# Kernel tuning notes

Hardware: AMD Instinct MI355X
Metric: run time of the kernel (lower is better)

The kernel has to match this reference:

```python
import jax, jax.numpy as jnp
import numpy as np

B, S, D, F, E, K = 2, 1024, 2048, 8192, 4, 2  # batch, seq, d_model, d_ff, n_experts, top_k


def setup_inputs() -> dict:
    key = jax.random.key(0)
    k0, k1, k2, k3, k4 = jax.random.split(key, 5)
    scaled = lambda k, shape, fan_in: (jax.random.normal(k, shape, jnp.float32) * (fan_in ** -0.5))
    return {
        "x": jax.random.normal(k0, (B, S, D), jnp.float32),
        "Wr": scaled(k1, (D, E), D),          # router (gating_layer.gate) weight
        "Wg": scaled(k2, (E, D, F), D),        # stacked expert gate_proj weights
        "Wu": scaled(k3, (E, D, F), D),        # stacked expert up_proj weights
        "Wd": scaled(k4, (E, F, D), F),        # stacked expert down_proj weights
    }


def reference(x, Wr, Wg, Wu, Wd):
    # Router: softmax over expert logits, take top-k values + indices
    probs = jax.nn.softmax(x @ Wr, axis=-1)                 # [B,S,E]
    gate_vals, gate_idx = jax.lax.top_k(probs, K)           # [B,S,K] each

    # Dense per-expert SwiGLU MLP for EVERY token (faithful to the original loop)
    g = jax.nn.silu(jnp.einsum('bsd,edf->bsef', x, Wg))     # [B,S,E,F]
    u = jnp.einsum('bsd,edf->bsef', x, Wu)                  # [B,S,E,F]
    eo = jnp.einsum('bsef,efd->bsed', g * u, Wd)            # [B,S,E,D]

    # Gather the top-k experts per token, scale by gate values, sum (combine)
    idx = jnp.broadcast_to(gate_idx[..., None], (B, S, K, D))
    sel = jnp.take_along_axis(eo, idx, axis=2)              # [B,S,K,D]
    return (sel * gate_vals[..., None]).sum(axis=2)         # [B,S,D]
```

## Files before the change

kernel.cpp:

```cpp
#include <hip/hip_runtime.h>
#include <stdint.h>


#define T_TOK 2048
#define DM    2048
#define FF    8192
#define DF    ((size_t)DM * FF)

typedef unsigned short u16;
typedef short short8 __attribute__((ext_vector_type(8)));
typedef float f32x4  __attribute__((ext_vector_type(4)));

#define GLL16(g, l) __builtin_amdgcn_global_load_lds( \
    (const __attribute__((address_space(1))) void*)(g), \
    (__attribute__((address_space(3))) void*)(l), 16, 0, 0)

__device__ __forceinline__ u16 f2bf(float f) {
  uint32_t x = __float_as_uint(f);
  x += 0x7fffu + ((x >> 16) & 1u);
  return (u16)(x >> 16);
}

__global__ __launch_bounds__(256) void router_kernel(
    const float* __restrict__ x, const float* __restrict__ Wr,
    int* __restrict__ counts, int* __restrict__ tok, float* __restrict__ gate)
{
  int t = blockIdx.x * 4 + (threadIdx.x >> 6);
  int l = threadIdx.x & 63;
  const float* xr = x + (size_t)t * DM;
  const float4* wr4 = (const float4*)Wr;
  float a0 = 0.f, a1 = 0.f, a2 = 0.f, a3 = 0.f;
  for (int d = l; d < DM; d += 64) {
    float xv = xr[d];
    float4 w = wr4[d];
    a0 += xv * w.x; a1 += xv * w.y; a2 += xv * w.z; a3 += xv * w.w;
  }
  #pragma unroll
  for (int off = 32; off > 0; off >>= 1) {
    a0 += __shfl_down(a0, off);
    a1 += __shfl_down(a1, off);
    a2 += __shfl_down(a2, off);
    a3 += __shfl_down(a3, off);
  }
  if (l == 0) {
    float lg[4] = {a0, a1, a2, a3};
    float m = fmaxf(fmaxf(lg[0], lg[1]), fmaxf(lg[2], lg[3]));
    float p[4], s = 0.f;
    #pragma unroll
    for (int e = 0; e < 4; ++e) { p[e] = __expf(lg[e] - m); s += p[e]; }
    #pragma unroll
    for (int e = 0; e < 4; ++e) p[e] /= s;
    int i0 = 0;
    #pragma unroll
    for (int e = 1; e < 4; ++e) if (p[e] > p[i0]) i0 = e;
    int i1 = (i0 == 0) ? 1 : 0;
    #pragma unroll
    for (int e = 0; e < 4; ++e) if (e != i0 && p[e] > p[i1]) i1 = e;
    int s0 = atomicAdd(&counts[i0], 1);
    tok[i0 * T_TOK + s0] = t; gate[i0 * T_TOK + s0] = p[i0];
    int s1 = atomicAdd(&counts[i1], 1);
    tok[i1 * T_TOK + s1] = t; gate[i1 * T_TOK + s1] = p[i1];
  }
}

__global__ __launch_bounds__(256) void gather_kernel(
    const float* __restrict__ x, const int* __restrict__ counts,
    const int* __restrict__ tok, u16* __restrict__ Xe)
{
  int e = blockIdx.x >> 11;
  int slot = blockIdx.x & (T_TOK - 1);
  if (slot >= counts[e]) return;
  int t = tok[e * T_TOK + slot];
  const float4* src = (const float4*)(x + (size_t)t * DM);
  u16* dst = Xe + ((size_t)e * T_TOK + slot) * DM;
  int i = threadIdx.x;
  float4 a = src[i * 2], b = src[i * 2 + 1];
  union { u16 h[8]; uint4 q; } v;
  v.h[0] = f2bf(a.x); v.h[1] = f2bf(a.y); v.h[2] = f2bf(a.z); v.h[3] = f2bf(a.w);
  v.h[4] = f2bf(b.x); v.h[5] = f2bf(b.y); v.h[6] = f2bf(b.z); v.h[7] = f2bf(b.w);
  *(uint4*)(dst + i * 8) = v.q;
}

__global__ __launch_bounds__(256) void trans_cvt_all(
    const float* __restrict__ Wg, const float* __restrict__ Wu, const float* __restrict__ Wd,
    u16* __restrict__ Wgt, u16* __restrict__ Wut, u16* __restrict__ Wdt)
{
  int j = blockIdx.y;
  const float* src; u16* dst; int R, C, clog;
  if (j < 4)      { src = Wg + (size_t)j * DF;       dst = Wgt + (size_t)j * DF;       R = DM; C = FF; clog = 7; }
  else if (j < 8) { src = Wu + (size_t)(j - 4) * DF; dst = Wut + (size_t)(j - 4) * DF; R = DM; C = FF; clog = 7; }
  else            { src = Wd + (size_t)(j - 8) * DF; dst = Wdt + (size_t)(j - 8) * DF; R = FF; C = DM; clog = 5; }
  int bx = blockIdx.x;
  int c0 = (bx & ((1 << clog) - 1)) * 64;
  int r0 = (bx >> clog) * 64;

  __shared__ float tile[64][65];
  int tid = threadIdx.x;
  int tc = tid & 63, tr = tid >> 6;
  #pragma unroll
  for (int i = 0; i < 16; ++i) {
    int row = i * 4 + tr;
    tile[row][tc] = src[(size_t)(r0 + row) * C + c0 + tc];
  }
  __syncthreads();
  int wr = tid & 15, rr = tid >> 4;
  #pragma unroll
  for (int i = 0; i < 4; ++i) {
    int row = i * 16 + rr;
    ushort4 v;
    v.x = f2bf(tile[wr * 4 + 0][row]);
    v.y = f2bf(tile[wr * 4 + 1][row]);
    v.z = f2bf(tile[wr * 4 + 2][row]);
    v.w = f2bf(tile[wr * 4 + 3][row]);
    *(ushort4*)&dst[(size_t)(c0 + row) * R + r0 + wr * 4] = v;
  }
}

__global__ __launch_bounds__(256, 2) void gemm12_kernel(
    const u16* __restrict__ XeB, const u16* __restrict__ WgtB, const u16* __restrict__ WutB,
    u16* __restrict__ HB, const int* __restrict__ counts)
{
  const int e  = blockIdx.y >> 4;
  const int rb = blockIdx.y & 15;
  const int cnt = counts[e];
  if (rb * 128 >= cnt) return;
  const u16* A  = XeB + (size_t)e * T_TOK * DM;
  const u16* Bg = WgtB + (size_t)e * DF;
  const u16* Bu = WutB + (size_t)e * DF;
  u16* H = HB + (size_t)e * T_TOK * FF;

  __shared__ __align__(16) u16 As[128 * 64];
  __shared__ __align__(16) u16 Bgs[128 * 64];
  __shared__ __align__(16) u16 Bus[128 * 64];
  const int tid = threadIdx.x, l = tid & 63, w = tid >> 6;
  const int wm = w & 1, wn = w >> 1;
  const int cg = (l & 7) ^ (l >> 3);
  const u16* ap[4]; const u16* bgp[4]; const u16* bup[4];
  const u16* la[4]; const u16* lbg[4]; const u16* lbu[4];
  #pragma unroll
  for (int j = 0; j < 4; ++j) {
    int r0 = (w * 4 + j) * 8;
    int row = r0 + (l >> 3);
    ap[j]  = A  + (size_t)(rb * 128 + row) * DM + cg * 8;
    bgp[j] = Bg + (size_t)(blockIdx.x * 128 + row) * DM + cg * 8;
    bup[j] = Bu + (size_t)(blockIdx.x * 128 + row) * DM + cg * 8;
    la[j]  = As  + r0 * 64;
    lbg[j] = Bgs + r0 * 64;
    lbu[j] = Bus + r0 * 64;
  }
  int fm[4], fn[4];
  #pragma unroll
  for (int i = 0; i < 4; ++i) {
    fm[i] = (wm * 64 + i * 16 + (l & 15)) * 64;
    fn[i] = (wn * 64 + i * 16 + (l & 15)) * 64;
  }
  f32x4 accg[4][4] = {};
  f32x4 accu[4][4] = {};
  for (int kt = 0; kt < DM / 64; ++kt) {
    #pragma unroll
    for (int j = 0; j < 4; ++j) {
      GLL16(ap[j]  + kt * 64, la[j]);
      GLL16(bgp[j] + kt * 64, lbg[j]);
      GLL16(bup[j] + kt * 64, lbu[j]);
    }
    __syncthreads();
    #pragma unroll
    for (int kk = 0; kk < 2; ++kk) {
      const int c2 = ((kk * 4 + (l >> 4)) ^ (l & 7)) * 8;
      short8 af[4], bgf[4], buf_[4];
      #pragma unroll
      for (int i = 0; i < 4; ++i) af[i]   = *(const short8*)&As[fm[i] + c2];
      #pragma unroll
      for (int i = 0; i < 4; ++i) bgf[i]  = *(const short8*)&Bgs[fn[i] + c2];
      #pragma unroll
      for (int i = 0; i < 4; ++i) buf_[i] = *(const short8*)&Bus[fn[i] + c2];
      #pragma unroll
      for (int mt = 0; mt < 4; ++mt)
        #pragma unroll
        for (int nt = 0; nt < 4; ++nt) {
          accg[mt][nt] = __builtin_amdgcn_mfma_f32_16x16x32_bf16(af[mt], bgf[nt],  accg[mt][nt], 0, 0, 0);
          accu[mt][nt] = __builtin_amdgcn_mfma_f32_16x16x32_bf16(af[mt], buf_[nt], accu[mt][nt], 0, 0, 0);
        }
    }
    __syncthreads();
  }
  const int rbase = rb * 128 + wm * 64 + ((l >> 4) << 2);
  const int cbase = blockIdx.x * 128 + wn * 64 + (l & 15);
  #pragma unroll
  for (int mt = 0; mt < 4; ++mt) {
    #pragma unroll
    for (int i = 0; i < 4; ++i) {
      int r = rbase + mt * 16 + i;
      u16* hrow = H + (size_t)r * FF + cbase;
      #pragma unroll
      for (int nt = 0; nt < 4; ++nt) {
        float g = accg[mt][nt][i], u = accu[mt][nt][i];
        float h = (g / (1.f + __expf(-g))) * u;
        hrow[nt * 16] = f2bf(h);
      }
    }
  }
}

__global__ __launch_bounds__(256, 2) void gemm3_kernel(
    const u16* __restrict__ HB, const u16* __restrict__ WdtB,
    float* __restrict__ out, const int* __restrict__ counts,
    const int* __restrict__ tokB, const float* __restrict__ gateB)
{
  const int e  = blockIdx.y >> 4;
  const int rb = blockIdx.y & 15;
  const int cnt = counts[e];
  if (rb * 128 >= cnt) return;
  const u16* A = HB + (size_t)e * T_TOK * FF;
  const u16* B = WdtB + (size_t)e * DF;
  const int* tokd = tokB + e * T_TOK;
  const float* gated = gateB + e * T_TOK;
  const int kt0 = blockIdx.z * 64, kt1 = kt0 + 64;

  __shared__ __align__(16) u16 As[128 * 64];
  __shared__ __align__(16) u16 Bs[128 * 64];
  const int tid = threadIdx.x, l = tid & 63, w = tid >> 6;
  const int wm = w & 1, wn = w >> 1;
  const int cg = (l & 7) ^ (l >> 3);
  const u16* ap[4]; const u16* bp[4]; const u16* la[4]; const u16* lb[4];
  #pragma unroll
  for (int j = 0; j < 4; ++j) {
    int r0 = (w * 4 + j) * 8;
    int row = r0 + (l >> 3);
    ap[j] = A + (size_t)(rb * 128 + row) * FF + cg * 8;
    bp[j] = B + (size_t)(blockIdx.x * 128 + row) * FF + cg * 8;
    la[j] = As + r0 * 64;
    lb[j] = Bs + r0 * 64;
  }
  int fm[4], fn[4];
  #pragma unroll
  for (int i = 0; i < 4; ++i) {
    fm[i] = (wm * 64 + i * 16 + (l & 15)) * 64;
    fn[i] = (wn * 64 + i * 16 + (l & 15)) * 64;
  }
  f32x4 acc[4][4] = {};
  for (int kt = kt0; kt < kt1; ++kt) {
    #pragma unroll
    for (int j = 0; j < 4; ++j) {
      GLL16(ap[j] + kt * 64, la[j]);
      GLL16(bp[j] + kt * 64, lb[j]);
    }
    __syncthreads();
    #pragma unroll
    for (int kk = 0; kk < 2; ++kk) {
      const int c2 = ((kk * 4 + (l >> 4)) ^ (l & 7)) * 8;
      short8 af[4], bf[4];
      #pragma unroll
      for (int i = 0; i < 4; ++i) af[i] = *(const short8*)&As[fm[i] + c2];
      #pragma unroll
      for (int i = 0; i < 4; ++i) bf[i] = *(const short8*)&Bs[fn[i] + c2];
      #pragma unroll
      for (int mt = 0; mt < 4; ++mt)
        #pragma unroll
        for (int nt = 0; nt < 4; ++nt)
          acc[mt][nt] = __builtin_amdgcn_mfma_f32_16x16x32_bf16(af[mt], bf[nt], acc[mt][nt], 0, 0, 0);
    }
    __syncthreads();
  }
  const int rbase = rb * 128 + wm * 64 + ((l >> 4) << 2);
  const int cbase = blockIdx.x * 128 + wn * 64 + (l & 15);
  #pragma unroll
  for (int mt = 0; mt < 4; ++mt) {
    #pragma unroll
    for (int i = 0; i < 4; ++i) {
      int r = rbase + mt * 16 + i;
      if (r < cnt) {
        int t = tokd[r];
        float gv = gated[r];
        float* orow = out + (size_t)t * DM + cbase;
        #pragma unroll
        for (int nt = 0; nt < 4; ++nt)
          atomicAdd(orow + nt * 16, acc[mt][nt][i] * gv);
      }
    }
  }
}

extern "C" void kernel_launch(void* const* d_in, const int* in_sizes, int n_in,
                              void* d_out, int out_size, void* d_ws, size_t ws_size,
                              hipStream_t stream) {
  (void)in_sizes; (void)n_in; (void)out_size; (void)ws_size;
  const float* x  = (const float*)d_in[0];
  const float* Wr = (const float*)d_in[1];
  const float* Wg = (const float*)d_in[2];
  const float* Wu = (const float*)d_in[3];
  const float* Wd = (const float*)d_in[4];
  float* out = (float*)d_out;

  char* ws = (char*)d_ws;
  int*   counts = (int*)(ws);
  int*   tok    = (int*)(ws + 1024);
  float* gate   = (float*)(ws + 1024 + 4 * T_TOK * 4);
  u16*   Xe     = (u16*)(ws + 1024 + 2 * 4 * T_TOK * 4);
  u16*   Wgt    = Xe  + (size_t)4 * T_TOK * DM;
  u16*   Wut    = Wgt + 4 * DF;
  u16*   Wdt    = Wut + 4 * DF;
  u16*   H      = Wdt + 4 * DF;

  hipMemsetAsync(out, 0, (size_t)T_TOK * DM * sizeof(float), stream);
  hipMemsetAsync(counts, 0, 4 * sizeof(int), stream);

  router_kernel<<<T_TOK / 4, 256, 0, stream>>>(x, Wr, counts, tok, gate);
  gather_kernel<<<4 * T_TOK, 256, 0, stream>>>(x, counts, tok, Xe);
  trans_cvt_all<<<dim3(4096, 12), 256, 0, stream>>>(Wg, Wu, Wd, Wgt, Wut, Wdt);
  gemm12_kernel<<<dim3(FF / 128, 64), 256, 0, stream>>>(Xe, Wgt, Wut, H, counts);
  gemm3_kernel<<<dim3(DM / 128, 64, 2), 256, 0, stream>>>(H, Wdt, out, counts, tok, gate);
}
```

Baseline: 1.333 ms.

## Triple-buffer GEMM LDS tiles with 8-wave blocks and vectorize weight transpose

```diff
diff --git a/kernel.cpp b/kernel.cpp
--- a/kernel.cpp
+++ b/kernel.cpp
@@ -14,6 +14,12 @@
 #define GLL16(g, l) __builtin_amdgcn_global_load_lds( \
     (const __attribute__((address_space(1))) void*)(g), \
     (__attribute__((address_space(3))) void*)(l), 16, 0, 0)
+
+#define BARRIER() do { asm volatile("" ::: "memory"); __builtin_amdgcn_s_barrier(); asm volatile("" ::: "memory"); } while (0)
+#define LGK0()    do { asm volatile("s_waitcnt lgkmcnt(0)" ::: "memory"); __builtin_amdgcn_sched_barrier(0); } while (0)
+#define VMW(N)    asm volatile("s_waitcnt vmcnt(" #N ")" ::: "memory")
+#define PRIO1()   __builtin_amdgcn_s_setprio(1)
+#define PRIO0()   __builtin_amdgcn_s_setprio(0)
 
 __device__ __forceinline__ u16 f2bf(float f) {
   uint32_t x = __float_as_uint(f);
@@ -94,29 +100,28 @@
   int c0 = (bx & ((1 << clog) - 1)) * 64;
   int r0 = (bx >> clog) * 64;
 
-  __shared__ float tile[64][65];
+  __shared__ float tile[64][68];
   int tid = threadIdx.x;
-  int tc = tid & 63, tr = tid >> 6;
-  #pragma unroll
-  for (int i = 0; i < 16; ++i) {
-    int row = i * 4 + tr;
-    tile[row][tc] = src[(size_t)(r0 + row) * C + c0 + tc];
+  const float4* s4 = (const float4*)(src + (size_t)r0 * C + c0);
+  const int cq = C >> 2;
+  #pragma unroll
+  for (int k2 = 0; k2 < 4; ++k2) {
+    int f = tid + 256 * k2;
+    int row = f >> 4, c4 = f & 15;
+    float4 v = s4[(size_t)row * cq + c4];
+    *(float4*)&tile[row][c4 * 4] = v;
   }
   __syncthreads();
-  int wr = tid & 15, rr = tid >> 4;
-  #pragma unroll
-  for (int i = 0; i < 4; ++i) {
-    int row = i * 16 + rr;
-    ushort4 v;
-    v.x = f2bf(tile[wr * 4 + 0][row]);
-    v.y = f2bf(tile[wr * 4 + 1][row]);
-    v.z = f2bf(tile[wr * 4 + 2][row]);
-    v.w = f2bf(tile[wr * 4 + 3][row]);
-    *(ushort4*)&dst[(size_t)(c0 + row) * R + r0 + wr * 4] = v;
-  }
-}
-
-__global__ __launch_bounds__(256, 2) void gemm12_kernel(
+  int ro = tid >> 2, seg = tid & 3;
+  union { u16 h[16]; uint4 q[2]; } v;
+  #pragma unroll
+  for (int i = 0; i < 16; ++i) v.h[i] = f2bf(tile[seg * 16 + i][ro]);
+  u16* drow = dst + (size_t)(c0 + ro) * R + r0 + seg * 16;
+  *(uint4*)(drow)     = v.q[0];
+  *(uint4*)(drow + 8) = v.q[1];
+}
+
+__global__ __launch_bounds__(512, 2) void gemm12_kernel(
     const u16* __restrict__ XeB, const u16* __restrict__ WgtB, const u16* __restrict__ WutB,
     u16* __restrict__ HB, const int* __restrict__ counts)
 {
@@ -124,85 +129,103 @@
   const int rb = blockIdx.y & 15;
   const int cnt = counts[e];
   if (rb * 128 >= cnt) return;
-  const u16* A  = XeB + (size_t)e * T_TOK * DM;
-  const u16* Bg = WgtB + (size_t)e * DF;
-  const u16* Bu = WutB + (size_t)e * DF;
+  const u16* Ag  = XeB  + (size_t)e * T_TOK * DM + (size_t)rb * 128 * DM;
+  const u16* Bgg = WgtB + (size_t)e * DF + (size_t)blockIdx.x * 128 * DM;
+  const u16* Bug = WutB + (size_t)e * DF + (size_t)blockIdx.x * 128 * DM;
   u16* H = HB + (size_t)e * T_TOK * FF;
 
-  __shared__ __align__(16) u16 As[128 * 64];
-  __shared__ __align__(16) u16 Bgs[128 * 64];
-  __shared__ __align__(16) u16 Bus[128 * 64];
+  __shared__ __align__(16) u16 ldsT[3][3][128 * 64];
+
   const int tid = threadIdx.x, l = tid & 63, w = tid >> 6;
   const int wm = w & 1, wn = w >> 1;
   const int cg = (l & 7) ^ (l >> 3);
-  const u16* ap[4]; const u16* bgp[4]; const u16* bup[4];
-  const u16* la[4]; const u16* lbg[4]; const u16* lbu[4];
-  #pragma unroll
-  for (int j = 0; j < 4; ++j) {
-    int r0 = (w * 4 + j) * 8;
-    int row = r0 + (l >> 3);
-    ap[j]  = A  + (size_t)(rb * 128 + row) * DM + cg * 8;
-    bgp[j] = Bg + (size_t)(blockIdx.x * 128 + row) * DM + cg * 8;
-    bup[j] = Bu + (size_t)(blockIdx.x * 128 + row) * DM + cg * 8;
-    la[j]  = As  + r0 * 64;
-    lbg[j] = Bgs + r0 * 64;
-    lbu[j] = Bus + r0 * 64;
-  }
-  int fm[4], fn[4];
-  #pragma unroll
-  for (int i = 0; i < 4; ++i) {
-    fm[i] = (wm * 64 + i * 16 + (l & 15)) * 64;
-    fn[i] = (wn * 64 + i * 16 + (l & 15)) * 64;
-  }
-  f32x4 accg[4][4] = {};
-  f32x4 accu[4][4] = {};
-  for (int kt = 0; kt < DM / 64; ++kt) {
-    #pragma unroll
-    for (int j = 0; j < 4; ++j) {
-      GLL16(ap[j]  + kt * 64, la[j]);
-      GLL16(bgp[j] + kt * 64, lbg[j]);
-      GLL16(bup[j] + kt * 64, lbu[j]);
-    }
-    __syncthreads();
-    #pragma unroll
-    for (int kk = 0; kk < 2; ++kk) {
-      const int c2 = ((kk * 4 + (l >> 4)) ^ (l & 7)) * 8;
-      short8 af[4], bgf[4], buf_[4];
+  const size_t so0 = (size_t)(w * 16 + (l >> 3)) * DM + cg * 8;
+  const size_t so1 = so0 + (size_t)8 * DM;
+  const int lo0 = w * 1024;
+  const int lo1 = lo0 + 512;
+
+  int fmA[4], fnB[2], c2k[2];
+  #pragma unroll
+  for (int m = 0; m < 4; ++m) fmA[m] = (wm * 64 + m * 16 + (l & 15)) * 64;
+  #pragma unroll
+  for (int n = 0; n < 2; ++n) fnB[n] = (wn * 32 + n * 16 + (l & 15)) * 64;
+  c2k[0] = ((l >> 4) ^ (l & 7)) * 8;
+  c2k[1] = ((4 + (l >> 4)) ^ (l & 7)) * 8;
+
+  f32x4 accg[4][2] = {};
+  f32x4 accu[4][2] = {};
+
+  #define G12_STAGE(ti, which, srcp) do { \
+    u16* d_ = &ldsT[(ti) % 3][which][0]; \
+    GLL16((srcp) + (size_t)(ti) * 64 + so0, d_ + lo0); \
+    GLL16((srcp) + (size_t)(ti) * 64 + so1, d_ + lo1); } while (0)
+
+  G12_STAGE(0, 0, Ag); G12_STAGE(0, 1, Bgg);
+  G12_STAGE(0, 2, Bug);
+  G12_STAGE(1, 0, Ag); G12_STAGE(1, 1, Bgg);
+  G12_STAGE(1, 2, Bug);
+  VMW(8);
+  BARRIER();
+
+  #define G12_KTILE(T, ISSUE, KA, KB) do { \
+    const u16* a_  = &ldsT[(T) % 3][0][0]; \
+    const u16* bg_ = &ldsT[(T) % 3][1][0]; \
+    const u16* bu_ = &ldsT[(T) % 3][2][0]; \
+    short8 af[2][4], bgf[2][2], buf2[2][2]; \
+    _Pragma("unroll") \
+    for (int kk = 0; kk < 2; ++kk) { \
+      _Pragma("unroll") \
+      for (int m = 0; m < 4; ++m) af[kk][m] = *(const short8*)&a_[fmA[m] + c2k[kk]]; \
+      _Pragma("unroll") \
+      for (int n = 0; n < 2; ++n) bgf[kk][n] = *(const short8*)&bg_[fnB[n] + c2k[kk]]; \
+    } \
+    if (ISSUE) { G12_STAGE((T) + 2, 0, Ag); G12_STAGE((T) + 2, 1, Bgg); } \
+    BARRIER(); LGK0(); PRIO1(); \
+    _Pragma("unroll") \
+    for (int kk = 0; kk < 2; ++kk) \
+      _Pragma("unroll") \
+      for (int m = 0; m < 4; ++m) \
+        _Pragma("unroll") \
+        for (int n = 0; n < 2; ++n) \
+          accg[m][n] = __builtin_amdgcn_mfma_f32_16x16x32_bf16(af[kk][m], bgf[kk][n], accg[m][n], 0, 0, 0); \
+    PRIO0(); VMW(KA); BARRIER(); \
+    _Pragma("unroll") \
+    for (int kk = 0; kk < 2; ++kk) { \
+      _Pragma("unroll") \
+      for (int n = 0; n < 2; ++n) buf2[kk][n] = *(const short8*)&bu_[fnB[n] + c2k[kk]]; \
+    } \
+    if (ISSUE) { G12_STAGE((T) + 2, 2, Bug); } \
+    BARRIER(); LGK0(); PRIO1(); \
+    _Pragma("unroll") \
+    for (int kk = 0; kk < 2; ++kk) \
+      _Pragma("unroll") \
+      for (int m = 0; m < 4; ++m) \
+        _Pragma("unroll") \
+        for (int n = 0; n < 2; ++n) \
+          accu[m][n] = __builtin_amdgcn_mfma_f32_16x16x32_bf16(af[kk][m], buf2[kk][n], accu[m][n], 0, 0, 0); \
+    PRIO0(); VMW(KB); BARRIER(); \
+  } while (0)
+
+  for (int t = 0; t < 30; ++t) G12_KTILE(t, 1, 10, 8);
+  G12_KTILE(30, 0, 6, 2);
+  G12_KTILE(31, 0, 0, 0);
+
+  const int rloc = rb * 128 + wm * 64 + ((l >> 4) << 2);
+  const int cb   = blockIdx.x * 128 + wn * 32 + (l & 15);
+  #pragma unroll
+  for (int m = 0; m < 4; ++m)
+    #pragma unroll
+    for (int i = 0; i < 4; ++i) {
+      u16* hrow = H + (size_t)(rloc + m * 16 + i) * FF + cb;
       #pragma unroll
-      for (int i = 0; i < 4; ++i) af[i]   = *(const short8*)&As[fm[i] + c2];
-      #pragma unroll
-      for (int i = 0; i < 4; ++i) bgf[i]  = *(const short8*)&Bgs[fn[i] + c2];
-      #pragma unroll
-      for (int i = 0; i < 4; ++i) buf_[i] = *(const short8*)&Bus[fn[i] + c2];
-      #pragma unroll
-      for (int mt = 0; mt < 4; ++mt)
-        #pragma unroll
-        for (int nt = 0; nt < 4; ++nt) {
-          accg[mt][nt] = __builtin_amdgcn_mfma_f32_16x16x32_bf16(af[mt], bgf[nt],  accg[mt][nt], 0, 0, 0);
-          accu[mt][nt] = __builtin_amdgcn_mfma_f32_16x16x32_bf16(af[mt], buf_[nt], accu[mt][nt], 0, 0, 0);
-        }
-    }
-    __syncthreads();
-  }
-  const int rbase = rb * 128 + wm * 64 + ((l >> 4) << 2);
-  const int cbase = blockIdx.x * 128 + wn * 64 + (l & 15);
-  #pragma unroll
-  for (int mt = 0; mt < 4; ++mt) {
-    #pragma unroll
-    for (int i = 0; i < 4; ++i) {
-      int r = rbase + mt * 16 + i;
-      u16* hrow = H + (size_t)r * FF + cbase;
-      #pragma unroll
-      for (int nt = 0; nt < 4; ++nt) {
-        float g = accg[mt][nt][i], u = accu[mt][nt][i];
-        float h = (g / (1.f + __expf(-g))) * u;
-        hrow[nt * 16] = f2bf(h);
+      for (int n = 0; n < 2; ++n) {
+        float g = accg[m][n][i], u = accu[m][n][i];
+        hrow[n * 16] = f2bf((g / (1.f + __expf(-g))) * u);
       }
     }
-  }
-}
-
-__global__ __launch_bounds__(256, 2) void gemm3_kernel(
+}
+
+__global__ __launch_bounds__(512, 2) void gemm3_kernel(
     const u16* __restrict__ HB, const u16* __restrict__ WdtB,
     float* __restrict__ out, const int* __restrict__ counts,
     const int* __restrict__ tokB, const float* __restrict__ gateB)
@@ -211,74 +234,93 @@
   const int rb = blockIdx.y & 15;
   const int cnt = counts[e];
   if (rb * 128 >= cnt) return;
-  const u16* A = HB + (size_t)e * T_TOK * FF;
-  const u16* B = WdtB + (size_t)e * DF;
+  const u16* Ag = HB   + (size_t)e * T_TOK * FF + (size_t)rb * 128 * FF;
+  const u16* Bgp = WdtB + (size_t)e * DF + (size_t)blockIdx.x * 256 * FF;
   const int* tokd = tokB + e * T_TOK;
   const float* gated = gateB + e * T_TOK;
-  const int kt0 = blockIdx.z * 64, kt1 = kt0 + 64;
-
-  __shared__ __align__(16) u16 As[128 * 64];
-  __shared__ __align__(16) u16 Bs[128 * 64];
+
+  __shared__ __align__(16) u16 ldsA[3][128 * 64];
+  __shared__ __align__(16) u16 ldsB[3][256 * 64];
+
   const int tid = threadIdx.x, l = tid & 63, w = tid >> 6;
   const int wm = w & 1, wn = w >> 1;
   const int cg = (l & 7) ^ (l >> 3);
-  const u16* ap[4]; const u16* bp[4]; const u16* la[4]; const u16* lb[4];
-  #pragma unroll
-  for (int j = 0; j < 4; ++j) {
-    int r0 = (w * 4 + j) * 8;
-    int row = r0 + (l >> 3);
-    ap[j] = A + (size_t)(rb * 128 + row) * FF + cg * 8;
-    bp[j] = B + (size_t)(blockIdx.x * 128 + row) * FF + cg * 8;
-    la[j] = As + r0 * 64;
-    lb[j] = Bs + r0 * 64;
-  }
-  int fm[4], fn[4];
-  #pragma unroll
-  for (int i = 0; i < 4; ++i) {
-    fm[i] = (wm * 64 + i * 16 + (l & 15)) * 64;
-    fn[i] = (wn * 64 + i * 16 + (l & 15)) * 64;
-  }
+  const size_t so0 = (size_t)(w * 16 + (l >> 3)) * FF + cg * 8;
+  const size_t so1 = so0 + (size_t)8 * FF;
+  const int lo0 = w * 1024, lo1 = lo0 + 512;
+
+  int fmA[4], fnB_[4], c2k[2];
+  #pragma unroll
+  for (int m = 0; m < 4; ++m) fmA[m] = (wm * 64 + m * 16 + (l & 15)) * 64;
+  #pragma unroll
+  for (int n = 0; n < 4; ++n) fnB_[n] = (wn * 64 + n * 16 + (l & 15)) * 64;
+  c2k[0] = ((l >> 4) ^ (l & 7)) * 8;
+  c2k[1] = ((4 + (l >> 4)) ^ (l & 7)) * 8;
+
   f32x4 acc[4][4] = {};
-  for (int kt = kt0; kt < kt1; ++kt) {
-    #pragma unroll
-    for (int j = 0; j < 4; ++j) {
-      GLL16(ap[j] + kt * 64, la[j]);
-      GLL16(bp[j] + kt * 64, lb[j]);
-    }
-    __syncthreads();
-    #pragma unroll
-    for (int kk = 0; kk < 2; ++kk) {
-      const int c2 = ((kk * 4 + (l >> 4)) ^ (l & 7)) * 8;
-      short8 af[4], bf[4];
-      #pragma unroll
-      for (int i = 0; i < 4; ++i) af[i] = *(const short8*)&As[fm[i] + c2];
-      #pragma unroll
-      for (int i = 0; i < 4; ++i) bf[i] = *(const short8*)&Bs[fn[i] + c2];
-      #pragma unroll
-      for (int mt = 0; mt < 4; ++mt)
+
+  #define G3_STAGE_A(ti) do { u16* d_ = &ldsA[(ti) % 3][0]; \
+    GLL16(Ag + (size_t)(ti) * 64 + so0, d_ + lo0); \
+    GLL16(Ag + (size_t)(ti) * 64 + so1, d_ + lo1); } while (0)
+  #define G3_STAGE_B(ti, half) do { u16* d_ = &ldsB[(ti) % 3][(half) * (128 * 64)]; \
+    GLL16(Bgp + (size_t)(half) * 128 * FF + (size_t)(ti) * 64 + so0, d_ + lo0); \
+    GLL16(Bgp + (size_t)(half) * 128 * FF + (size_t)(ti) * 64 + so1, d_ + lo1); } while (0)
+
+  G3_STAGE_A(0); G3_STAGE_B(0, 0);
+  G3_STAGE_B(0, 1);
+  G3_STAGE_A(1); G3_STAGE_B(1, 0);
+  G3_STAGE_B(1, 1);
+  VMW(6);
+  BARRIER();
+
+  #define G3_KTILE(T, ISSUE, KB) do { \
+    const u16* a_ = &ldsA[(T) % 3][0]; const u16* b_ = &ldsB[(T) % 3][0]; \
+    short8 af[4], bf[4]; \
+    _Pragma("unroll") \
+    for (int m = 0; m < 4; ++m) af[m] = *(const short8*)&a_[fmA[m] + c2k[0]]; \
+    _Pragma("unroll") \
+    for (int n = 0; n < 4; ++n) bf[n] = *(const short8*)&b_[fnB_[n] + c2k[0]]; \
+    if (ISSUE) { G3_STAGE_A((T) + 2); G3_STAGE_B((T) + 2, 0); } \
+    BARRIER(); LGK0(); PRIO1(); \
+    _Pragma("unroll") \
+    for (int m = 0; m < 4; ++m) \
+      _Pragma("unroll") \
+      for (int n = 0; n < 4; ++n) \
+        acc[m][n] = __builtin_amdgcn_mfma_f32_16x16x32_bf16(af[m], bf[n], acc[m][n], 0, 0, 0); \
+    PRIO0(); BARRIER(); \
+    _Pragma("unroll") \
+    for (int m = 0; m < 4; ++m) af[m] = *(const short8*)&a_[fmA[m] + c2k[1]]; \
+    _Pragma("unroll") \
+    for (int n = 0; n < 4; ++n) bf[n] = *(const short8*)&b_[fnB_[n] + c2k[1]]; \
+    if (ISSUE) { G3_STAGE_B((T) + 2, 1); } \
+    BARRIER(); LGK0(); PRIO1(); \
+    _Pragma("unroll") \
+    for (int m = 0; m < 4; ++m) \
+      _Pragma("unroll") \
+      for (int n = 0; n < 4; ++n) \
+        acc[m][n] = __builtin_amdgcn_mfma_f32_16x16x32_bf16(af[m], bf[n], acc[m][n], 0, 0, 0); \
+    PRIO0(); VMW(KB); BARRIER(); \
+  } while (0)
+
+  for (int t = 0; t < 126; ++t) G3_KTILE(t, 1, 6);
+  G3_KTILE(126, 0, 0);
+  G3_KTILE(127, 0, 0);
+
+  const int rloc = wm * 64 + ((l >> 4) << 2);
+  const int cb   = blockIdx.x * 256 + wn * 64 + (l & 15);
+  #pragma unroll
+  for (int m = 0; m < 4; ++m)
+    #pragma unroll
+    for (int i = 0; i < 4; ++i) {
+      int r = rb * 128 + rloc + m * 16 + i;
+      if (r < cnt) {
+        float gv = gated[r];
+        float* orow = out + (size_t)tokd[r] * DM + cb;
         #pragma unroll
-        for (int nt = 0; nt < 4; ++nt)
-          acc[mt][nt] = __builtin_amdgcn_mfma_f32_16x16x32_bf16(af[mt], bf[nt], acc[mt][nt], 0, 0, 0);
-    }
-    __syncthreads();
-  }
-  const int rbase = rb * 128 + wm * 64 + ((l >> 4) << 2);
-  const int cbase = blockIdx.x * 128 + wn * 64 + (l & 15);
-  #pragma unroll
-  for (int mt = 0; mt < 4; ++mt) {
-    #pragma unroll
-    for (int i = 0; i < 4; ++i) {
-      int r = rbase + mt * 16 + i;
-      if (r < cnt) {
-        int t = tokd[r];
-        float gv = gated[r];
-        float* orow = out + (size_t)t * DM + cbase;
-        #pragma unroll
-        for (int nt = 0; nt < 4; ++nt)
-          atomicAdd(orow + nt * 16, acc[mt][nt][i] * gv);
+        for (int n = 0; n < 4; ++n)
+          atomicAdd(orow + n * 16, acc[m][n][i] * gv);
       }
     }
-  }
 }
 
 extern "C" void kernel_launch(void* const* d_in, const int* in_sizes, int n_in,
@@ -308,6 +350,6 @@
   router_kernel<<<T_TOK / 4, 256, 0, stream>>>(x, Wr, counts, tok, gate);
   gather_kernel<<<4 * T_TOK, 256, 0, stream>>>(x, counts, tok, Xe);
   trans_cvt_all<<<dim3(4096, 12), 256, 0, stream>>>(Wg, Wu, Wd, Wgt, Wut, Wdt);
-  gemm12_kernel<<<dim3(FF / 128, 64), 256, 0, stream>>>(Xe, Wgt, Wut, H, counts);
-  gemm3_kernel<<<dim3(DM / 128, 64, 2), 256, 0, stream>>>(H, Wdt, out, counts, tok, gate);
-}
+  gemm12_kernel<<<dim3(FF / 128, 64), 512, 0, stream>>>(Xe, Wgt, Wut, H, counts);
+  gemm3_kernel<<<dim3(DM / 256, 64), 512, 0, stream>>>(H, Wdt, out, counts, tok, gate);
+}
```

New measurement: 1.431 ms. 7.3% more time.
